# Performance work log

Hardware: AMD Instinct MI355X
Metric: run time of the kernel (lower is better)

Reference implementation:

```python
import jax, jax.numpy as jnp
import numpy as np

N_NODES = 50000


def _sage_max(x, src, dst, W_l, b_l, W_r):
    # gather neighbor (source) features, scatter-max to destination nodes
    msgs = x[src]                                   # [E, F]
    agg = jax.ops.segment_max(msgs, dst, num_segments=N_NODES)  # [N, F], -inf for empty
    agg = jnp.where(jnp.isneginf(agg), 0.0, agg)    # PyG fills isolated nodes with 0
    return agg @ W_l + b_l + x @ W_r                # lin_l(aggr) + lin_r(x)


def setup_inputs() -> dict:
    key = jax.random.key(0)
    ks = jax.random.split(key, 9)
    F_IN, H, OUT, E, EL = 128, 256, 32, 800000, 200000
    x = jax.random.normal(ks[0], (N_NODES, F_IN), dtype=jnp.float32)
    edge_index = jax.random.randint(ks[1], (2, E), 0, N_NODES, dtype=jnp.int64)
    edge_label_index = jax.random.randint(ks[2], (2, EL), 0, N_NODES, dtype=jnp.int64)
    s1 = 1.0 / np.sqrt(F_IN)
    s2 = 1.0 / np.sqrt(H)
    W1_l = jax.random.normal(ks[3], (F_IN, H), dtype=jnp.float32) * s1
    b1 = jnp.zeros((H,), dtype=jnp.float32)
    W1_r = jax.random.normal(ks[4], (F_IN, H), dtype=jnp.float32) * s1
    W2_l = jax.random.normal(ks[5], (H, OUT), dtype=jnp.float32) * s2
    b2 = jnp.zeros((OUT,), dtype=jnp.float32)
    W2_r = jax.random.normal(ks[6], (H, OUT), dtype=jnp.float32) * s2
    return {"x": x, "edge_index": edge_index, "edge_label_index": edge_label_index,
            "W1_l": W1_l, "b1": b1, "W1_r": W1_r,
            "W2_l": W2_l, "b2": b2, "W2_r": W2_r}


def reference(x, edge_index, edge_label_index, W1_l, b1, W1_r, W2_l, b2, W2_r):
    src, dst = edge_index[0], edge_index[1]
    # encode (eval mode: dropout is identity)
    h = jax.nn.relu(_sage_max(x, src, dst, W1_l, b1, W1_r))
    z = _sage_max(h, src, dst, W2_l, b2, W2_r)       # [N, 32]
    # decode: dot product between endpoint embeddings
    s = z[edge_label_index[0]]
    d = z[edge_label_index[1]]
    return jnp.sum(s * d, axis=-1)                   # [E_label]
```

## Files before the change

### kernel.cpp

```cpp
#include <hip/hip_runtime.h>
#include <hip/hip_bf16.h>
#include <math.h>

#define N_NODES 50000
#define NBKT 196
#define BSH 8
#define TILE2 4096
#define CAP 64
#define P2CAP 5888
#define SCAN_FLAG 0x40000000

typedef __attribute__((ext_vector_type(8))) short short8;
typedef __attribute__((ext_vector_type(4))) float f32x4;

static __device__ __forceinline__ float b2f(unsigned int u16) {
    union { unsigned int i; float f; } c; c.i = u16 << 16; return c.f;
}
static __device__ __forceinline__ unsigned int fbits(float f) {
    union { float f; unsigned int i; } c; c.f = f; return c.i;
}
static __device__ __forceinline__ unsigned short f2b_rne(float f) {
    unsigned int u = fbits(f);
    u += 0x7fff + ((u >> 16) & 1);
    return (unsigned short)(u >> 16);
}

static __device__ __forceinline__ unsigned char quant8(float v) {
    int q = (int)(v * 15.9375f + 0.5f);
    return (unsigned char)min(q, 255);
}

static __device__ __forceinline__ unsigned char q8x(float v) {
    int q = __float2int_rn(v * 21.333334f) + 128;
    return (unsigned char)min(max(q, 0), 255);
}

static __device__ __forceinline__ short8 dq8(uint2 v8) {
    short8 r;
#pragma unroll
    for (int bi = 0; bi < 4; ++bi)
        r[bi] = (short)f2b_rne((float)((v8.x >> (8 * bi)) & 255u) * 0.0627451f);
#pragma unroll
    for (int bi = 0; bi < 4; ++bi)
        r[4 + bi] = (short)f2b_rne((float)((v8.y >> (8 * bi)) & 255u) * 0.0627451f);
    return r;
}

#define BYTEMAX16(V) do {                                                             \
    m[0]  = max(m[0],  (int)((V).x & 0xFF));                                          \
    m[1]  = max(m[1],  (int)(((V).x >> 8) & 0xFF));                                   \
    m[2]  = max(m[2],  (int)(((V).x >> 16) & 0xFF));                                  \
    m[3]  = max(m[3],  (int)((V).x >> 24));                                           \
    m[4]  = max(m[4],  (int)((V).y & 0xFF));                                          \
    m[5]  = max(m[5],  (int)(((V).y >> 8) & 0xFF));                                   \
    m[6]  = max(m[6],  (int)(((V).y >> 16) & 0xFF));                                  \
    m[7]  = max(m[7],  (int)((V).y >> 24));                                           \
    m[8]  = max(m[8],  (int)((V).z & 0xFF));                                          \
    m[9]  = max(m[9],  (int)(((V).z >> 8) & 0xFF));                                   \
    m[10] = max(m[10], (int)(((V).z >> 16) & 0xFF));                                  \
    m[11] = max(m[11], (int)((V).z >> 24));                                           \
    m[12] = max(m[12], (int)((V).w & 0xFF));                                          \
    m[13] = max(m[13], (int)(((V).w >> 8) & 0xFF));                                   \
    m[14] = max(m[14], (int)(((V).w >> 16) & 0xFF));                                  \
    m[15] = max(m[15], (int)((V).w >> 24));                                           \
} while (0)


__global__ __launch_bounds__(256) void k_prepbin(
        const float* __restrict__ x, unsigned short* __restrict__ xb,
        unsigned char* __restrict__ x8,
        const float* __restrict__ W1l, const float* __restrict__ W1r, unsigned short* __restrict__ wt1,
        const float* __restrict__ W2l, const float* __restrict__ W2r, unsigned short* __restrict__ wt2,
        float* __restrict__ zb,
        const int* __restrict__ src, const int* __restrict__ dst, int E,
        uint2* __restrict__ tmp, int* __restrict__ cnts, int ntile) {
    __shared__ int cnt[256], sstart[256], lcur[256];
    __shared__ uint2 stage[TILE2];
    const int CX = (N_NODES * 128 / 4) / 256;
    const int CW = CX + 320;
    const int CZ = CW + 1563;
    int b = blockIdx.x, t = threadIdx.x;
    if (b < CX) {
        int i = b * 256 + t;
        float4 v = *(const float4*)(x + (size_t)i * 4);
        ushort4 o;
        o.x = f2b_rne(v.x); o.y = f2b_rne(v.y); o.z = f2b_rne(v.z); o.w = f2b_rne(v.w);
        *(ushort4*)(xb + (size_t)i * 4) = o;
        uchar4 c8;
        c8.x = q8x(v.x); c8.y = q8x(v.y); c8.z = q8x(v.z); c8.w = q8x(v.w);
        *(uchar4*)(x8 + (size_t)i * 4) = c8;
    } else if (b < CX + 256) {
        int i = (b - CX) * 256 + t;
        int n = i >> 8, k = i & 255;
        float v = (k < 128) ? W1l[(size_t)k * 256 + n] : W1r[(size_t)(k - 128) * 256 + n];
        wt1[(size_t)n * 256 + k] = f2b_rne(v);
    } else if (b < CW) {
        int i = (b - CX - 256) * 256 + t;
        int n = i >> 9, k = i & 511;
        float v = (k < 256) ? W2l[(size_t)k * 32 + n] : W2r[(size_t)(k - 256) * 32 + n];
        wt2[(size_t)n * 512 + k] = f2b_rne(v);
    } else if (b < CZ) {
        int i = (b - CW) * 256 + t;
        if (i < 400000) ((float4*)zb)[i] = (float4){0.f, 0.f, 0.f, 0.f};
    } else {
        int tb = b - CZ;
        int e0 = tb * TILE2;
        int tilecnt = min(TILE2, E - e0);
        if (tilecnt <= 0) return;
        cnt[t] = 0;
        __syncthreads();
        if (tilecnt == TILE2) {
            for (int i = 4 * t; i < TILE2; i += 1024) {
                int4 d = *(const int4*)(dst + e0 + i);
                atomicAdd(&cnt[d.x >> BSH], 1);
                atomicAdd(&cnt[d.y >> BSH], 1);
                atomicAdd(&cnt[d.z >> BSH], 1);
                atomicAdd(&cnt[d.w >> BSH], 1);
            }
        } else {
            for (int i = t; i < tilecnt; i += 256)
                atomicAdd(&cnt[dst[e0 + i] >> BSH], 1);
        }
        __syncthreads();
        int cv = cnt[t];
        sstart[t] = cv;
        __syncthreads();
        for (int off = 1; off < 256; off <<= 1) {
            int add = (t >= off) ? sstart[t - off] : 0;
            __syncthreads();
            sstart[t] += add;
            __syncthreads();
        }
        int mystart = sstart[t] - cv;
        __syncthreads();
        sstart[t] = mystart;
        lcur[t] = mystart;
        __syncthreads();
        if (tilecnt == TILE2) {
            for (int i = 4 * t; i < TILE2; i += 1024) {
                int4 d = *(const int4*)(dst + e0 + i);
                int4 s = *(const int4*)(src + e0 + i);
                int q0 = atomicAdd(&lcur[d.x >> BSH], 1); stage[q0] = (uint2){(unsigned)s.x, (unsigned)d.x};
                int q1 = atomicAdd(&lcur[d.y >> BSH], 1); stage[q1] = (uint2){(unsigned)s.y, (unsigned)d.y};
                int q2 = atomicAdd(&lcur[d.z >> BSH], 1); stage[q2] = (uint2){(unsigned)s.z, (unsigned)d.z};
                int q3 = atomicAdd(&lcur[d.w >> BSH], 1); stage[q3] = (uint2){(unsigned)s.w, (unsigned)d.w};
            }
        } else {
            for (int i = t; i < tilecnt; i += 256) {
                int d = dst[e0 + i];
                int s = src[e0 + i];
                int q = atomicAdd(&lcur[d >> BSH], 1);
                uint2 p; p.x = (unsigned)s; p.y = (unsigned)d;
                stage[q] = p;
            }
        }
        __syncthreads();
        if (t < NBKT) cnts[(size_t)t * ntile + tb] = cnt[t];
        for (int i = t; i < tilecnt; i += 256) {
            uint2 p = stage[i];
            int bk = (int)(p.y >> BSH);
            tmp[((size_t)bk * ntile + tb) * CAP + (i - sstart[bk])] = p;
        }
    }
}


__global__ __launch_bounds__(256) void k_bin2(const uint2* __restrict__ tmp,
        const int* __restrict__ cnts, int* __restrict__ pub,
        int* __restrict__ rowptr, int* __restrict__ esrc, int N, int E, int ntile) {
    __shared__ int sc[256], toff[260], nodecnt[256], lcur[256];
    __shared__ int stage[P2CAP];
    __shared__ int shsum[4];
    int k = blockIdx.x, t = threadIdx.x;
    int grp = t >> 5, lane32 = t & 31;

    int c = (t < ntile) ? cnts[(size_t)k * ntile + t] : 0;
    sc[t] = c;
    __syncthreads();
    for (int off = 1; off < 256; off <<= 1) {
        int add = (t >= off) ? sc[t - off] : 0;
        __syncthreads();
        sc[t] += add;
        __syncthreads();
    }
    if (t < ntile) toff[t] = sc[t] - c;
    if (t == 255) toff[ntile] = sc[255];
    __syncthreads();
    int total = toff[ntile];

    if (t == 255) atomicExch(&pub[k], SCAN_FLAG | total);
    int v = 0;
    if (t < k) {
        int val;
        do { val = atomicOr(&pub[t], 0); } while (!(val & SCAN_FLAG) || (val & 0x80000000));
        v = val & (SCAN_FLAG - 1);
    }
#pragma unroll
    for (int off = 32; off >= 1; off >>= 1) v += __shfl_xor(v, off);
    if ((t & 63) == 0) shsum[t >> 6] = v;
    nodecnt[t] = 0;
    __syncthreads();
    int base = shsum[0] + shsum[1] + shsum[2] + shsum[3];

    for (int tile = grp; tile < ntile; tile += 8) {
        int tc = toff[tile + 1] - toff[tile];
        for (int e = lane32; e < tc; e += 32) {
            uint2 p = tmp[((size_t)k * ntile + tile) * CAP + e];
            atomicAdd(&nodecnt[(int)p.y & 255], 1);
        }
    }
    __syncthreads();

    int nc = nodecnt[t];
    sc[t] = nc;
    __syncthreads();
    for (int off = 1; off < 256; off <<= 1) {
        int add = (t >= off) ? sc[t - off] : 0;
        __syncthreads();
        sc[t] += add;
        __syncthreads();
    }
    int ex = sc[t] - nc;
    int node = (k << BSH) + t;
    if (node < N) rowptr[node] = base + ex;
    if (node == N) rowptr[N] = E;
    lcur[t] = ex;
    __syncthreads();

    if (total <= P2CAP) {
        for (int tile = grp; tile < ntile; tile += 8) {
            int tc = toff[tile + 1] - toff[tile];
            for (int e = lane32; e < tc; e += 32) {
                uint2 p = tmp[((size_t)k * ntile + tile) * CAP + e];
                int q = atomicAdd(&lcur[(int)p.y & 255], 1);
                stage[q] = (int)p.x;
            }
        }
        __syncthreads();
        for (int i = t; i < total; i += 256)
            esrc[base + i] = stage[i];
    } else {
        for (int tile = grp; tile < ntile; tile += 8) {
            int tc = toff[tile + 1] - toff[tile];
            for (int e = lane32; e < tc; e += 32) {
                uint2 p = tmp[((size_t)k * ntile + tile) * CAP + e];
                int q = atomicAdd(&lcur[(int)p.y & 255], 1);
                esrc[base + q] = (int)p.x;
            }
        }
    }
}


__global__ __launch_bounds__(256) void k_seg_max1(const unsigned char* __restrict__ feat8,
        const int* __restrict__ rowptr, const int* __restrict__ esrc,
        unsigned short* __restrict__ out) {
    int w = threadIdx.x >> 6, t = threadIdx.x & 63;
    int n = blockIdx.x * 4 + w;
    int lane8 = t & 7, sub = t >> 3;
    int beg = rowptr[n], end = rowptr[n + 1];
    int m[16];
#pragma unroll
    for (int k = 0; k < 16; ++k) m[k] = 0;
    for (int base = beg; base < end; base += 64) {
        int cnt = min(64, end - base);
        int vidx = (base + t < end) ? __builtin_nontemporal_load(&esrc[base + t]) : 0;
        for (int j = 0; j < cnt; j += 32) {
            int lim = cnt - j;
            if (lim > 16) {
                uint4 v[4];
#pragma unroll
                for (int u = 0; u < 4; ++u) {
                    int e = min(j + 8 * u + sub, cnt - 1);
                    int s = __shfl(vidx, e);
                    v[u] = *(const uint4*)(feat8 + (size_t)s * 128 + lane8 * 16);
                }
#pragma unroll
                for (int u = 0; u < 4; ++u) BYTEMAX16(v[u]);
            } else if (lim > 8) {
                uint4 v[2];
#pragma unroll
                for (int u = 0; u < 2; ++u) {
                    int e = min(j + 8 * u + sub, cnt - 1);
                    int s = __shfl(vidx, e);
                    v[u] = *(const uint4*)(feat8 + (size_t)s * 128 + lane8 * 16);
                }
#pragma unroll
                for (int u = 0; u < 2; ++u) BYTEMAX16(v[u]);
            } else {
                int e = min(j + sub, cnt - 1);
                int s = __shfl(vidx, e);
                uint4 v0 = *(const uint4*)(feat8 + (size_t)s * 128 + lane8 * 16);
                BYTEMAX16(v0);
            }
        }
    }
#pragma unroll
    for (int k = 0; k < 16; ++k) {
        m[k] = max(m[k], __shfl_xor(m[k], 8));
        m[k] = max(m[k], __shfl_xor(m[k], 16));
        m[k] = max(m[k], __shfl_xor(m[k], 32));
    }
    if (sub == 0) {
        unsigned int pk[8];
#pragma unroll
        for (int k = 0; k < 8; ++k) {
            float f0 = (beg == end) ? 0.f : (float)(m[2 * k]     - 128) * 0.046875f;
            float f1 = (beg == end) ? 0.f : (float)(m[2 * k + 1] - 128) * 0.046875f;
            pk[k] = (fbits(f0) >> 16) | (fbits(f1) & 0xffff0000u);
        }
        uint4 a, b;
        a.x = pk[0]; a.y = pk[1]; a.z = pk[2]; a.w = pk[3];
        b.x = pk[4]; b.y = pk[5]; b.z = pk[6]; b.w = pk[7];
        *(uint4*)(out + (size_t)n * 128 + lane8 * 16) = a;
        *(uint4*)(out + (size_t)n * 128 + lane8 * 16 + 8) = b;
    }
}


__global__ __launch_bounds__(256) void k_seg_max2(const unsigned char* __restrict__ feat8,
        const int* __restrict__ rowptr, const int* __restrict__ esrc,
        unsigned char* __restrict__ out8) {
    int w = threadIdx.x >> 6, t = threadIdx.x & 63;
    int n = blockIdx.x * 4 + w;
    int lane16 = t & 15, sub = t >> 4;
    int beg = rowptr[n], end = rowptr[n + 1];
    int m[16];
#pragma unroll
    for (int k = 0; k < 16; ++k) m[k] = 0;
    for (int base = beg; base < end; base += 64) {
        int cnt = min(64, end - base);
        int vidx = (base + t < end) ? __builtin_nontemporal_load(&esrc[base + t]) : 0;
        for (int j = 0; j < cnt; j += 32) {
            int lim = cnt - j;
            if (lim > 16) {
                uint4 v[8];
#pragma unroll
                for (int u = 0; u < 8; ++u) {
                    int e = min(j + 4 * u + sub, cnt - 1);
                    int s = __shfl(vidx, e);
                    v[u] = *(const uint4*)(feat8 + (size_t)s * 256 + lane16 * 16);
                }
#pragma unroll
                for (int u = 0; u < 8; ++u) BYTEMAX16(v[u]);
            } else if (lim > 8) {
                uint4 v[4];
#pragma unroll
                for (int u = 0; u < 4; ++u) {
                    int e = min(j + 4 * u + sub, cnt - 1);
                    int s = __shfl(vidx, e);
                    v[u] = *(const uint4*)(feat8 + (size_t)s * 256 + lane16 * 16);
                }
#pragma unroll
                for (int u = 0; u < 4; ++u) BYTEMAX16(v[u]);
            } else {
                uint4 v[2];
#pragma unroll
                for (int u = 0; u < 2; ++u) {
                    int e = min(j + 4 * u + sub, cnt - 1);
                    int s = __shfl(vidx, e);
                    v[u] = *(const uint4*)(feat8 + (size_t)s * 256 + lane16 * 16);
                }
#pragma unroll
                for (int u = 0; u < 2; ++u) BYTEMAX16(v[u]);
            }
        }
    }
#pragma unroll
    for (int k = 0; k < 16; ++k) {
        m[k] = max(m[k], __shfl_xor(m[k], 16));
        m[k] = max(m[k], __shfl_xor(m[k], 32));
    }
    if (sub == 0) {
        uint4 p;
        p.x = m[0]  | (m[1]  << 8) | (m[2]  << 16) | (m[3]  << 24);
        p.y = m[4]  | (m[5]  << 8) | (m[6]  << 16) | (m[7]  << 24);
        p.z = m[8]  | (m[9]  << 8) | (m[10] << 16) | (m[11] << 24);
        p.w = m[12] | (m[13] << 8) | (m[14] << 16) | (m[15] << 24);
        *(uint4*)(out8 + (size_t)n * 256 + lane16 * 16) = p;
    }
}


#define STAGE(bi, K0) do {                                                            \
    const unsigned short* Ab_ = ((K0) < 128) ? A0 : A1;                               \
    int kab_ = ((K0) & 127) * 2;                                                      \
    int kbb_ = (K0) * 2;                                                              \
    _Pragma("unroll")                                                                 \
    for (int ii = 0; ii < 2; ++ii) {                                                  \
        int c_ = ii * 256 + tid;                                                      \
        int r_ = c_ >> 2, gs_ = (c_ & 3) ^ (r_ & 3);                                  \
        const char* ga_ = (const char*)Ab_ + (size_t)(m0 + r_) * 256 + kab_ + gs_ * 16; \
        __builtin_amdgcn_global_load_lds(                                             \
            (const __attribute__((address_space(1))) void*)ga_,                       \
            (__attribute__((address_space(3))) void*)((char*)(SH + (bi) * 4096) + (ii * 256 + (tid & ~63)) * 16), \
            16, 0, 0);                                                                \
        const char* gb_ = (const char*)WT + (size_t)(n0 + r_) * 512 + kbb_ + gs_ * 16; \
        __builtin_amdgcn_global_load_lds(                                             \
            (const __attribute__((address_space(1))) void*)gb_,                       \
            (__attribute__((address_space(3))) void*)((char*)(SH + 12288 + (bi) * 4096) + (ii * 256 + (tid & ~63)) * 16), \
            16, 0, 0);                                                                \
    }                                                                                 \
} while (0)

#define VMCNT8() asm volatile("s_waitcnt vmcnt(8)" ::: "memory")
#define VMCNT6() asm volatile("s_waitcnt vmcnt(6)" ::: "memory")
#define VMCNT4() asm volatile("s_waitcnt vmcnt(4)" ::: "memory")
#define VMCNT3() asm volatile("s_waitcnt vmcnt(3)" ::: "memory")
#define VMCNT0() asm volatile("s_waitcnt vmcnt(0)" ::: "memory")
#define SBAR() do { __builtin_amdgcn_sched_barrier(0); __builtin_amdgcn_s_barrier(); __builtin_amdgcn_sched_barrier(0); } while (0)

#define COMPUTE(bi) do {                                                              \
    const short* Asb_ = SH + (bi) * 4096;                                             \
    const short* Bsb_ = SH + 12288 + (bi) * 4096;                                     \
    short8 a_[4], b_[4];                                                              \
    _Pragma("unroll")                                                                 \
    for (int i = 0; i < 4; ++i) {                                                     \
        int r_ = wr * 64 + i * 16 + lane16;                                           \
        a_[i] = *(const short8*)((const char*)Asb_ + r_ * 64 + ((q ^ (r_ & 3)) << 4)); \
    }                                                                                 \
    _Pragma("unroll")                                                                 \
    for (int j = 0; j < 4; ++j) {                                                     \
        int c_ = wc * 64 + j * 16 + lane16;                                           \
        b_[j] = *(const short8*)((const char*)Bsb_ + c_ * 64 + ((q ^ (c_ & 3)) << 4)); \
    }                                                                                 \
    _Pragma("unroll")                                                                 \
    for (int i = 0; i < 4; ++i)                                                       \
        _Pragma("unroll")                                                             \
        for (int j = 0; j < 4; ++j)                                                   \
            acc[i][j] = __builtin_amdgcn_mfma_f32_16x16x32_bf16(a_[i], b_[j], acc[i][j], 0, 0, 0); \
} while (0)

__global__ __launch_bounds__(256) void k_lin1_mfma(
        const unsigned short* __restrict__ A0, const unsigned short* __restrict__ A1,
        const unsigned short* __restrict__ WT, const float* __restrict__ bias,
        const unsigned short* __restrict__ WT2, float* __restrict__ zpart,
        unsigned char* __restrict__ H8, int M) {
    __shared__ __align__(16) short SH[24576];
    short* Hs = SH;

    int tid = threadIdx.x;
    int m0 = blockIdx.y * 128, n0 = blockIdx.x * 128;
    int L = tid & 63, wv = tid >> 6;
    int wr = wv >> 1, wc = wv & 1;
    int lane16 = L & 15, q = L >> 4;

    f32x4 acc[4][4];
#pragma unroll
    for (int i = 0; i < 4; ++i)
#pragma unroll
        for (int j = 0; j < 4; ++j) acc[i][j] = (f32x4){0.f, 0.f, 0.f, 0.f};

    STAGE(0, 0);
    STAGE(1, 32);
    STAGE(2, 64);

    VMCNT8(); SBAR(); COMPUTE(0); SBAR(); STAGE(0, 96);
    VMCNT8(); SBAR(); COMPUTE(1); SBAR(); STAGE(1, 128);
    VMCNT8(); SBAR(); COMPUTE(2); SBAR(); STAGE(2, 160);
    VMCNT8(); SBAR(); COMPUTE(0); SBAR(); STAGE(0, 192);
    VMCNT8(); SBAR(); COMPUTE(1); SBAR(); STAGE(1, 224);
    VMCNT8(); SBAR(); COMPUTE(2);
    VMCNT4(); SBAR(); COMPUTE(0);
    VMCNT0(); SBAR(); COMPUTE(1);

    __syncthreads();

#pragma unroll
    for (int i = 0; i < 4; ++i) {
#pragma unroll
        for (int r = 0; r < 4; ++r) {
            int lrow = wr * 64 + i * 16 + q * 4 + r;
            int row = m0 + lrow;
#pragma unroll
            for (int j = 0; j < 4; ++j) {
                int lcol = wc * 64 + j * 16 + lane16;
                int col = n0 + lcol;
                float v = fmaxf(acc[i][j][r] + bias[col], 0.f);
                Hs[lrow * 136 + lcol] = (short)f2b_rne(v);
                if (row < M) H8[(size_t)row * 256 + col] = quant8(v);
            }
        }
    }
    __syncthreads();

    f32x4 acc2[2][2];
#pragma unroll
    for (int i = 0; i < 2; ++i)
#pragma unroll
        for (int j = 0; j < 2; ++j) acc2[i][j] = (f32x4){0.f, 0.f, 0.f, 0.f};
#pragma unroll
    for (int kk = 0; kk < 4; ++kk) {
        short8 a2[2], b2[2];
#pragma unroll
        for (int i = 0; i < 2; ++i)
            a2[i] = *(const short8*)&Hs[(wv * 32 + i * 16 + lane16) * 136 + kk * 32 + q * 8];
#pragma unroll
        for (int j = 0; j < 2; ++j)
            b2[j] = *(const short8*)(WT2 + (size_t)(j * 16 + lane16) * 512 + 256 + n0 + kk * 32 + q * 8);
#pragma unroll
        for (int i = 0; i < 2; ++i)
#pragma unroll
            for (int j = 0; j < 2; ++j)
                acc2[i][j] = __builtin_amdgcn_mfma_f32_16x16x32_bf16(a2[i], b2[j], acc2[i][j], 0, 0, 0);
    }
#pragma unroll
    for (int i = 0; i < 2; ++i) {
#pragma unroll
        for (int r = 0; r < 4; ++r) {
            int row = m0 + wv * 32 + i * 16 + q * 4 + r;
            if (row >= M) continue;
#pragma unroll
            for (int j = 0; j < 2; ++j) {
                int col = j * 16 + lane16;
                atomicAdd(&zpart[(size_t)row * 32 + col], acc2[i][j][r]);
            }
        }
    }
}


#define STAGE2(bi, T) do {                                                            \
    _Pragma("unroll")                                                                 \
    for (int ii = 0; ii < 2; ++ii) {                                                  \
        int off_ = (ii * 256 + tid) * 16;                                             \
        int r_ = off_ >> 6, c_ = off_ & 63;                                           \
        const char* ga_ = (const char*)A8 + (size_t)(m0 + r_) * 256 + (T) * 64 + c_;  \
        __builtin_amdgcn_global_load_lds(                                             \
            (const __attribute__((address_space(1))) void*)ga_,                       \
            (__attribute__((address_space(3))) void*)(SH8 + (bi) * 8192 + (ii * 256 + (tid & ~63)) * 16), \
            16, 0, 0);                                                                \
    }                                                                                 \
    {                                                                                 \
        int off_ = tid * 16;                                                          \
        int r_ = off_ >> 7, c_ = off_ & 127;                                          \
        const char* gb_ = (const char*)WT + (size_t)r_ * 1024 + (T) * 128 + c_;       \
        __builtin_amdgcn_global_load_lds(                                             \
            (const __attribute__((address_space(1))) void*)gb_,                       \
            (__attribute__((address_space(3))) void*)(SH8 + 24576 + (bi) * 4096 + (tid & ~63) * 16), \
            16, 0, 0);                                                                \
    }                                                                                 \
} while (0)

#define COMPUTE2(bi) do {                                                             \
    const unsigned char* As_ = (const unsigned char*)SH8 + (bi) * 8192;               \
    const char* Bs_ = SH8 + 24576 + (bi) * 4096;                                      \
    _Pragma("unroll")                                                                 \
    for (int kk = 0; kk < 64; kk += 32) {                                             \
        short8 a_[2], b_[2];                                                          \
        _Pragma("unroll")                                                             \
        for (int i = 0; i < 2; ++i) {                                                 \
            uint2 va_ = *(const uint2*)(As_ + (wv * 32 + i * 16 + lane16) * 64 + kk + q * 8); \
            a_[i] = dq8(va_);                                                         \
        }                                                                             \
        _Pragma("unroll")                                                             \
        for (int j = 0; j < 2; ++j)                                                   \
            b_[j] = *(const short8*)(Bs_ + (j * 16 + lane16) * 128 + (kk + q * 8) * 2); \
        _Pragma("unroll")                                                             \
        for (int i = 0; i < 2; ++i)                                                   \
            _Pragma("unroll")                                                         \
            for (int j = 0; j < 2; ++j)                                               \
                acc[i][j] = __builtin_amdgcn_mfma_f32_16x16x32_bf16(a_[i], b_[j], acc[i][j], 0, 0, 0); \
    }                                                                                 \
} while (0)

__global__ __launch_bounds__(256) void k_lin2_mfma(
        const unsigned char* __restrict__ A8,
        const unsigned short* __restrict__ WT, const float* __restrict__ bias,
        float* __restrict__ Z, int M) {
    __shared__ __align__(16) char SH8[36864];

    int tid = threadIdx.x;
    int m0 = blockIdx.x * 128;
    int L = tid & 63, wv = tid >> 6;
    int lane16 = L & 15, q = L >> 4;

    f32x4 acc[2][2];
#pragma unroll
    for (int i = 0; i < 2; ++i)
#pragma unroll
        for (int j = 0; j < 2; ++j) acc[i][j] = (f32x4){0.f, 0.f, 0.f, 0.f};

    STAGE2(0, 0);
    STAGE2(1, 1);
    STAGE2(2, 2);

    VMCNT6(); SBAR(); COMPUTE2(0); SBAR(); STAGE2(0, 3);
    VMCNT6(); SBAR(); COMPUTE2(1);
    VMCNT3(); SBAR(); COMPUTE2(2);
    VMCNT0(); SBAR(); COMPUTE2(0);

#pragma unroll
    for (int i = 0; i < 2; ++i) {
#pragma unroll
        for (int r = 0; r < 4; ++r) {
            int row = m0 + wv * 32 + i * 16 + q * 4 + r;
            if (row >= M) continue;
#pragma unroll
            for (int j = 0; j < 2; ++j) {
                int col = j * 16 + lane16;
                float zp = Z[(size_t)row * 32 + col];
                Z[(size_t)row * 32 + col] = acc[i][j][r] + bias[col] + zp;
            }
        }
    }
}


__global__ void k_decode(const float* __restrict__ z, const int* __restrict__ eli,
                         int EL, float* __restrict__ out) {
    int tid = blockIdx.x * blockDim.x + threadIdx.x;
    int e = tid >> 3, lane = tid & 7;
    if (e >= EL) return;
    int s = eli[e], d = eli[EL + e];
    float4 a = *((const float4*)(z + (size_t)s * 32) + lane);
    float4 b = *((const float4*)(z + (size_t)d * 32) + lane);
    float dot = a.x * b.x + a.y * b.y + a.z * b.z + a.w * b.w;
    dot += __shfl_xor(dot, 1);
    dot += __shfl_xor(dot, 2);
    dot += __shfl_xor(dot, 4);
    if (lane == 0) out[e] = dot;
}


extern "C" void kernel_launch(void* const* d_in, const int* in_sizes, int n_in,
                              void* d_out, int out_size, void* d_ws, size_t ws_size,
                              hipStream_t stream) {
    const float* x   = (const float*)d_in[0];
    const int*   ei  = (const int*)d_in[1];
    const int*   eli = (const int*)d_in[2];
    const float* W1l = (const float*)d_in[3];
    const float* b1  = (const float*)d_in[4];
    const float* W1r = (const float*)d_in[5];
    const float* W2l = (const float*)d_in[6];
    const float* b2  = (const float*)d_in[7];
    const float* W2r = (const float*)d_in[8];
    float* out = (float*)d_out;

    int N  = N_NODES;
    int E  = in_sizes[1] / 2;
    int EL = in_sizes[2] / 2;
    const int* src = ei;
    const int* dst = ei + E;

    char* ws = (char*)d_ws;
    size_t off = 0;
    auto alloc = [&](size_t bytes) -> void* {
        void* p = ws + off;
        off += (bytes + 255) & ~(size_t)255;
        return p;
    };
    unsigned short* xb   = (unsigned short*)alloc((size_t)N * 128 * 2);
    unsigned char*  x8   = (unsigned char*)alloc((size_t)N * 128);
    unsigned short* aggb = (unsigned short*)alloc((size_t)(N + 128) * 256 * 2);
    unsigned char*  h8   = (unsigned char*)alloc((size_t)N * 256);
    float* zbuf          = (float*)alloc((size_t)N * 32 * 4);
    unsigned short* wt1  = (unsigned short*)alloc(256 * 256 * 2);
    unsigned short* wt2  = (unsigned short*)alloc(32 * 512 * 2);
    int* rowptr   = (int*)alloc((size_t)(N + 1) * 4);
    int ntile     = (E + TILE2 - 1) / TILE2;
    int* cnts     = (int*)alloc((size_t)NBKT * ntile * 4);
    int* pub      = (int*)alloc(256 * 4);
    int* esrc     = (int*)alloc((size_t)E * 4);
    uint2* tmpp   = (uint2*)aggb;
    unsigned char* agg8 = (unsigned char*)aggb;

    const int tb = 256;
    const int CZ = 6250 + 320 + 1563;

    k_prepbin<<<CZ + ntile, tb, 0, stream>>>(x, xb, x8, W1l, W1r, wt1, W2l, W2r, wt2, zbuf,
                                             src, dst, E, tmpp, cnts, ntile);
    k_bin2<<<NBKT, tb, 0, stream>>>(tmpp, cnts, pub, rowptr, esrc, N, E, ntile);

    k_seg_max1<<<(N + 3) / 4, tb, 0, stream>>>(x8, rowptr, esrc, aggb);
    dim3 g1(2, (N + 127) / 128);
    k_lin1_mfma<<<g1, tb, 0, stream>>>(aggb, xb, wt1, b1, wt2, zbuf, h8, N);

    k_seg_max2<<<(N + 3) / 4, tb, 0, stream>>>(h8, rowptr, esrc, agg8);
    k_lin2_mfma<<<(N + 127) / 128, tb, 0, stream>>>(agg8, wt2, b2, zbuf, N);

    k_decode<<<(EL * 8 + 255) / 256, tb, 0, stream>>>(zbuf, eli, EL, out);
}
```

Measured before the change: 225.8 us.

## Store layer-1 aggregation as uint8 and dequantize inside the MFMA GEMM

The first segment-max kernel now writes the max-aggregated features as packed 8-bit codes instead of expanding them to bf16. The layer-1 GEMM loads those bytes into shared memory and dequantizes them to bf16 in registers before the MFMA for the first half of K. This halves the aggregation write and read traffic. In exchange, the GEMM pipeline goes from three-buffer staging with fine vmcnt waits to a simpler double-buffer scheme with full __syncthreads, which may expose load latency and adds dequantization ALU work per tile.

```diff
diff --git a/kernel.cpp b/kernel.cpp
--- a/kernel.cpp
+++ b/kernel.cpp
@@ -43,6 +43,17 @@
 #pragma unroll
     for (int bi = 0; bi < 4; ++bi)
         r[4 + bi] = (short)f2b_rne((float)((v8.y >> (8 * bi)) & 255u) * 0.0627451f);
+    return r;
+}
+
+static __device__ __forceinline__ short8 dq8x(uint2 v8) {
+    short8 r;
+#pragma unroll
+    for (int bi = 0; bi < 4; ++bi)
+        r[bi] = (short)f2b_rne((float)((int)((v8.x >> (8 * bi)) & 255u) - 128) * 0.046875f);
+#pragma unroll
+    for (int bi = 0; bi < 4; ++bi)
+        r[4 + bi] = (short)f2b_rne((float)((int)((v8.y >> (8 * bi)) & 255u) - 128) * 0.046875f);
     return r;
 }
 
@@ -254,7 +265,7 @@
 
 __global__ __launch_bounds__(256) void k_seg_max1(const unsigned char* __restrict__ feat8,
         const int* __restrict__ rowptr, const int* __restrict__ esrc,
-        unsigned short* __restrict__ out) {
+        unsigned char* __restrict__ out8) {
     int w = threadIdx.x >> 6, t = threadIdx.x & 63;
     int n = blockIdx.x * 4 + w;
     int lane8 = t & 7, sub = t >> 3;
@@ -302,18 +313,16 @@
         m[k] = max(m[k], __shfl_xor(m[k], 32));
     }
     if (sub == 0) {
-        unsigned int pk[8];
-#pragma unroll
-        for (int k = 0; k < 8; ++k) {
-            float f0 = (beg == end) ? 0.f : (float)(m[2 * k]     - 128) * 0.046875f;
-            float f1 = (beg == end) ? 0.f : (float)(m[2 * k + 1] - 128) * 0.046875f;
-            pk[k] = (fbits(f0) >> 16) | (fbits(f1) & 0xffff0000u);
-        }
-        uint4 a, b;
-        a.x = pk[0]; a.y = pk[1]; a.z = pk[2]; a.w = pk[3];
-        b.x = pk[4]; b.y = pk[5]; b.z = pk[6]; b.w = pk[7];
-        *(uint4*)(out + (size_t)n * 128 + lane8 * 16) = a;
-        *(uint4*)(out + (size_t)n * 128 + lane8 * 16 + 8) = b;
+        uint4 p;
+        if (beg == end) {
+            p.x = p.y = p.z = p.w = 0x80808080u;
+        } else {
+            p.x = m[0]  | (m[1]  << 8) | (m[2]  << 16) | (m[3]  << 24);
+            p.y = m[4]  | (m[5]  << 8) | (m[6]  << 16) | (m[7]  << 24);
+            p.z = m[8]  | (m[9]  << 8) | (m[10] << 16) | (m[11] << 24);
+            p.w = m[12] | (m[13] << 8) | (m[14] << 16) | (m[15] << 24);
+        }
+        *(uint4*)(out8 + (size_t)n * 128 + lane8 * 16) = p;
     }
 }
 
@@ -382,48 +391,48 @@
 }
 
 
-#define STAGE(bi, K0) do {                                                            \
-    const unsigned short* Ab_ = ((K0) < 128) ? A0 : A1;                               \
-    int kab_ = ((K0) & 127) * 2;                                                      \
-    int kbb_ = (K0) * 2;                                                              \
+#define VMCNT6() asm volatile("s_waitcnt vmcnt(6)" ::: "memory")
+#define VMCNT3() asm volatile("s_waitcnt vmcnt(3)" ::: "memory")
+#define VMCNT0() asm volatile("s_waitcnt vmcnt(0)" ::: "memory")
+#define SBAR() do { __builtin_amdgcn_sched_barrier(0); __builtin_amdgcn_s_barrier(); __builtin_amdgcn_sched_barrier(0); } while (0)
+
+#define L1_STAGE_A8(b, K0) do {                                                       \
+    int off_ = tid * 16;                                                              \
+    int r_ = off_ >> 5, c_ = off_ & 31;                                               \
+    const char* ga_ = (const char*)A0 + (size_t)(m0 + r_) * 128 + (K0) + c_;          \
+    __builtin_amdgcn_global_load_lds(                                                 \
+        (const __attribute__((address_space(1))) void*)ga_,                           \
+        (__attribute__((address_space(3))) void*)(SH8 + (b) * 8192 + (tid & ~63) * 16), \
+        16, 0, 0);                                                                    \
+} while (0)
+
+#define L1_STAGE_A16(b, K0) do {                                                      \
     _Pragma("unroll")                                                                 \
     for (int ii = 0; ii < 2; ++ii) {                                                  \
         int c_ = ii * 256 + tid;                                                      \
         int r_ = c_ >> 2, gs_ = (c_ & 3) ^ (r_ & 3);                                  \
-        const char* ga_ = (const char*)Ab_ + (size_t)(m0 + r_) * 256 + kab_ + gs_ * 16; \
+        const char* ga_ = (const char*)A1 + (size_t)(m0 + r_) * 256 + ((K0) - 128) * 2 + gs_ * 16; \
         __builtin_amdgcn_global_load_lds(                                             \
             (const __attribute__((address_space(1))) void*)ga_,                       \
-            (__attribute__((address_space(3))) void*)((char*)(SH + (bi) * 4096) + (ii * 256 + (tid & ~63)) * 16), \
+            (__attribute__((address_space(3))) void*)(SH8 + (b) * 8192 + (ii * 256 + (tid & ~63)) * 16), \
             16, 0, 0);                                                                \
-        const char* gb_ = (const char*)WT + (size_t)(n0 + r_) * 512 + kbb_ + gs_ * 16; \
+    }                                                                                 \
+} while (0)
+
+#define L1_STAGE_B(b, K0) do {                                                        \
+    _Pragma("unroll")                                                                 \
+    for (int ii = 0; ii < 2; ++ii) {                                                  \
+        int c_ = ii * 256 + tid;                                                      \
+        int r_ = c_ >> 2, gs_ = (c_ & 3) ^ (r_ & 3);                                  \
+        const char* gb_ = (const char*)WT + (size_t)(n0 + r_) * 512 + (K0) * 2 + gs_ * 16; \
         __builtin_amdgcn_global_load_lds(                                             \
             (const __attribute__((address_space(1))) void*)gb_,                       \
-            (__attribute__((address_space(3))) void*)((char*)(SH + 12288 + (bi) * 4096) + (ii * 256 + (tid & ~63)) * 16), \
+            (__attribute__((address_space(3))) void*)(SH8 + 16384 + (b) * 8192 + (ii * 256 + (tid & ~63)) * 16), \
             16, 0, 0);                                                                \
     }                                                                                 \
 } while (0)
 
-#define VMCNT8() asm volatile("s_waitcnt vmcnt(8)" ::: "memory")
-#define VMCNT6() asm volatile("s_waitcnt vmcnt(6)" ::: "memory")
-#define VMCNT4() asm volatile("s_waitcnt vmcnt(4)" ::: "memory")
-#define VMCNT3() asm volatile("s_waitcnt vmcnt(3)" ::: "memory")
-#define VMCNT0() asm volatile("s_waitcnt vmcnt(0)" ::: "memory")
-#define SBAR() do { __builtin_amdgcn_sched_barrier(0); __builtin_amdgcn_s_barrier(); __builtin_amdgcn_sched_barrier(0); } while (0)
-
-#define COMPUTE(bi) do {                                                              \
-    const short* Asb_ = SH + (bi) * 4096;                                             \
-    const short* Bsb_ = SH + 12288 + (bi) * 4096;                                     \
-    short8 a_[4], b_[4];                                                              \
-    _Pragma("unroll")                                                                 \
-    for (int i = 0; i < 4; ++i) {                                                     \
-        int r_ = wr * 64 + i * 16 + lane16;                                           \
-        a_[i] = *(const short8*)((const char*)Asb_ + r_ * 64 + ((q ^ (r_ & 3)) << 4)); \
-    }                                                                                 \
-    _Pragma("unroll")                                                                 \
-    for (int j = 0; j < 4; ++j) {                                                     \
-        int c_ = wc * 64 + j * 16 + lane16;                                           \
-        b_[j] = *(const short8*)((const char*)Bsb_ + c_ * 64 + ((q ^ (c_ & 3)) << 4)); \
-    }                                                                                 \
+#define L1_MFMA16(a_, b_) do {                                                        \
     _Pragma("unroll")                                                                 \
     for (int i = 0; i < 4; ++i)                                                       \
         _Pragma("unroll")                                                             \
@@ -431,13 +440,48 @@
             acc[i][j] = __builtin_amdgcn_mfma_f32_16x16x32_bf16(a_[i], b_[j], acc[i][j], 0, 0, 0); \
 } while (0)
 
+#define L1_COMPUTE8(b) do {                                                           \
+    const char* Asb_ = SH8 + (b) * 8192;                                              \
+    const char* Bsb_ = SH8 + 16384 + (b) * 8192;                                      \
+    short8 a_[4], b_[4];                                                              \
+    _Pragma("unroll")                                                                 \
+    for (int i = 0; i < 4; ++i) {                                                     \
+        int r_ = wr * 64 + i * 16 + lane16;                                           \
+        uint2 va_ = *(const uint2*)(Asb_ + r_ * 32 + q * 8);                          \
+        a_[i] = dq8x(va_);                                                            \
+    }                                                                                 \
+    _Pragma("unroll")                                                                 \
+    for (int j = 0; j < 4; ++j) {                                                     \
+        int c_ = wc * 64 + j * 16 + lane16;                                           \
+        b_[j] = *(const short8*)(Bsb_ + c_ * 64 + ((q ^ (c_ & 3)) << 4));             \
+    }                                                                                 \
+    L1_MFMA16(a_, b_);                                                                \
+} while (0)
+
+#define L1_COMPUTE16(b) do {                                                          \
+    const char* Asb_ = SH8 + (b) * 8192;                                              \
+    const char* Bsb_ = SH8 + 16384 + (b) * 8192;                                      \
+    short8 a_[4], b_[4];                                                              \
+    _Pragma("unroll")                                                                 \
+    for (int i = 0; i < 4; ++i) {                                                     \
+        int r_ = wr * 64 + i * 16 + lane16;                                           \
+        a_[i] = *(const short8*)(Asb_ + r_ * 64 + ((q ^ (r_ & 3)) << 4));             \
+    }                                                                                 \
+    _Pragma("unroll")                                                                 \
+    for (int j = 0; j < 4; ++j) {                                                     \
+        int c_ = wc * 64 + j * 16 + lane16;                                           \
+        b_[j] = *(const short8*)(Bsb_ + c_ * 64 + ((q ^ (c_ & 3)) << 4));             \
+    }                                                                                 \
+    L1_MFMA16(a_, b_);                                                                \
+} while (0)
+
 __global__ __launch_bounds__(256) void k_lin1_mfma(
-        const unsigned short* __restrict__ A0, const unsigned short* __restrict__ A1,
+        const unsigned char* __restrict__ A0, const unsigned short* __restrict__ A1,
         const unsigned short* __restrict__ WT, const float* __restrict__ bias,
         const unsigned short* __restrict__ WT2, float* __restrict__ zpart,
         unsigned char* __restrict__ H8, int M) {
-    __shared__ __align__(16) short SH[24576];
-    short* Hs = SH;
+    __shared__ __align__(16) char SH8[34816];
+    short* Hs = (short*)SH8;
 
     int tid = threadIdx.x;
     int m0 = blockIdx.y * 128, n0 = blockIdx.x * 128;
@@ -451,19 +495,16 @@
 #pragma unroll
         for (int j = 0; j < 4; ++j) acc[i][j] = (f32x4){0.f, 0.f, 0.f, 0.f};
 
-    STAGE(0, 0);
-    STAGE(1, 32);
-    STAGE(2, 64);
-
-    VMCNT8(); SBAR(); COMPUTE(0); SBAR(); STAGE(0, 96);
-    VMCNT8(); SBAR(); COMPUTE(1); SBAR(); STAGE(1, 128);
-    VMCNT8(); SBAR(); COMPUTE(2); SBAR(); STAGE(2, 160);
-    VMCNT8(); SBAR(); COMPUTE(0); SBAR(); STAGE(0, 192);
-    VMCNT8(); SBAR(); COMPUTE(1); SBAR(); STAGE(1, 224);
-    VMCNT8(); SBAR(); COMPUTE(2);
-    VMCNT4(); SBAR(); COMPUTE(0);
-    VMCNT0(); SBAR(); COMPUTE(1);
-
+    L1_STAGE_A8(0, 0);   L1_STAGE_B(0, 0);
+    __syncthreads();
+    L1_STAGE_A8(1, 32);   L1_STAGE_B(1, 32);   L1_COMPUTE8(0);  __syncthreads();
+    L1_STAGE_A8(0, 64);   L1_STAGE_B(0, 64);   L1_COMPUTE8(1);  __syncthreads();
+    L1_STAGE_A8(1, 96);   L1_STAGE_B(1, 96);   L1_COMPUTE8(0);  __syncthreads();
+    L1_STAGE_A16(0, 128); L1_STAGE_B(0, 128);  L1_COMPUTE8(1);  __syncthreads();
+    L1_STAGE_A16(1, 160); L1_STAGE_B(1, 160);  L1_COMPUTE16(0); __syncthreads();
+    L1_STAGE_A16(0, 192); L1_STAGE_B(0, 192);  L1_COMPUTE16(1); __syncthreads();
+    L1_STAGE_A16(1, 224); L1_STAGE_B(1, 224);  L1_COMPUTE16(0); __syncthreads();
+    L1_COMPUTE16(1);
     __syncthreads();
 
 #pragma unroll
@@ -663,7 +704,8 @@
     int* pub      = (int*)alloc(256 * 4);
     int* esrc     = (int*)alloc((size_t)E * 4);
     uint2* tmpp   = (uint2*)aggb;
-    unsigned char* agg8 = (unsigned char*)aggb;
+    unsigned char* agg8_1 = (unsigned char*)aggb;
+    unsigned char* agg8_2 = (unsigned char*)aggb;
 
     const int tb = 256;
     const int CZ = 6250 + 320 + 1563;
@@ -672,12 +714,12 @@
                                              src, dst, E, tmpp, cnts, ntile);
     k_bin2<<<NBKT, tb, 0, stream>>>(tmpp, cnts, pub, rowptr, esrc, N, E, ntile);
 
-    k_seg_max1<<<(N + 3) / 4, tb, 0, stream>>>(x8, rowptr, esrc, aggb);
+    k_seg_max1<<<(N + 3) / 4, tb, 0, stream>>>(x8, rowptr, esrc, agg8_1);
     dim3 g1(2, (N + 127) / 128);
-    k_lin1_mfma<<<g1, tb, 0, stream>>>(aggb, xb, wt1, b1, wt2, zbuf, h8, N);
-
-    k_seg_max2<<<(N + 3) / 4, tb, 0, stream>>>(h8, rowptr, esrc, agg8);
-    k_lin2_mfma<<<(N + 127) / 128, tb, 0, stream>>>(agg8, wt2, b2, zbuf, N);
+    k_lin1_mfma<<<g1, tb, 0, stream>>>(agg8_1, xb, wt1, b1, wt2, zbuf, h8, N);
+
+    k_seg_max2<<<(N + 3) / 4, tb, 0, stream>>>(h8, rowptr, esrc, agg8_2);
+    k_lin2_mfma<<<(N + 127) / 128, tb, 0, stream>>>(agg8_2, wt2, b2, zbuf, N);
 
     k_decode<<<(EL * 8 + 255) / 256, tb, 0, stream>>>(zbuf, eli, EL, out);
 }
```

Measured after the change: 228.3 us. Within noise of the previous version (+1.1%).
